# Kernel tuning notes

Hardware: AMD Instinct MI355X
Metric: run time of the kernel (lower is better)

Reference implementation:

```python
import jax, jax.numpy as jnp
import numpy as np

ALPHA = 0.1


def setup_inputs() -> dict:
    key = jax.random.key(0)
    ks = jax.random.split(key, 12)
    B, C, Q, XD, YD, E, H = 4, 256, 256, 64, 32, 64, 128
    inp = {
        "x": jax.random.normal(ks[0], (B, C, XD), jnp.float32),
        "y": jax.random.normal(ks[1], (B, C, YD), jnp.float32),
        "r_c": jax.random.normal(ks[2], (B, C, C, E), jnp.float32),
        "r_q": jax.random.normal(ks[3], (B, C, Q, E), jnp.float32),
        "c_att_map": jax.random.uniform(ks[4], (B, C, C), jnp.float32),
        "q_att_map": jax.random.uniform(ks[5], (B, Q, C), jnp.float32),
        "W1": jax.random.normal(ks[6], (XD + YD + E, H), jnp.float32) * 0.05,
        "b1": jnp.zeros((H,), jnp.float32),
        "W2": jax.random.normal(ks[7], (H, H), jnp.float32) * 0.05,
        "b2": jnp.zeros((H,), jnp.float32),
        "W3": jax.random.normal(ks[8], (H, E), jnp.float32) * 0.05,
        "b3": jnp.zeros((E,), jnp.float32),
    }
    return inp


def reference(x, y, r_c, r_q, c_att_map, q_att_map, W1, b1, W2, b2, W3, b3):
    B, C = r_c.shape[0], r_c.shape[1]
    # tile x,y across an outer C axis and concat with pairwise embeddings
    xx = jnp.broadcast_to(x[:, None, :, :], (B, C, C, x.shape[-1]))
    yy = jnp.broadcast_to(y[:, None, :, :], (B, C, C, y.shape[-1]))
    h = jnp.concatenate([xx, yy, r_c], axis=-1)          # [B,C,C,XD+YD+E]
    h = jax.nn.relu(h @ W1 + b1)
    h = jax.nn.relu(h @ W2 + b2)
    U = h @ W3 + b3                                       # [B,C,C,E]
    # delta[b,k,i,e] = sum_j c_att_map[b,i,j] * U[b,k,j,e]
    delta_r_c = jnp.einsum("bij,bkje->bkie", c_att_map, U)
    delta_r_q = jnp.einsum("bqj,bkje->bkqe", q_att_map, U)
    next_r_c = r_c - ALPHA * delta_r_c
    next_r_q = r_q - ALPHA * delta_r_q
    return (next_r_c, next_r_q)
```

## Files before the change

### kernel.cpp

```cpp
#include <hip/hip_runtime.h>
#include <hip/hip_bf16.h>

typedef __attribute__((ext_vector_type(8))) short  short8;
typedef __attribute__((ext_vector_type(4))) short  short4v;
typedef __attribute__((ext_vector_type(4))) float  f32x4;

#define ALPHA 0.1f

__device__ __forceinline__ unsigned short f2bf(float f) {
    unsigned int u = __float_as_uint(f);
    u = (u + 0x7FFFu + ((u >> 16) & 1u)) >> 16;
    return (unsigned short)u;
}

__device__ __forceinline__ f32x4 mfma16(short8 a, short8 b, f32x4 c) {
    return __builtin_amdgcn_mfma_f32_16x16x32_bf16(a, b, c, 0, 0, 0);
}

#define WS_P     0u
#define WS_W1RT  524288u
#define WS_W2T   540672u
#define WS_W3T   573440u
#define WS_ATTC  589824u
#define WS_ATTQ  1114112u

__global__ __launch_bounds__(256) void prep_kernel(
    const float* __restrict__ x, const float* __restrict__ y,
    const float* __restrict__ cat, const float* __restrict__ qat,
    const float* __restrict__ W1, const float* __restrict__ b1,
    const float* __restrict__ W2, const float* __restrict__ W3,
    unsigned char* __restrict__ ws)
{
    const unsigned int blk = blockIdx.x, tid = threadIdx.x;
    float* P = (float*)(ws + WS_P);
    unsigned short* W1rT = (unsigned short*)(ws + WS_W1RT);
    unsigned short* W2T  = (unsigned short*)(ws + WS_W2T);
    unsigned short* W3T  = (unsigned short*)(ws + WS_W3T);
    unsigned short* AC   = (unsigned short*)(ws + WS_ATTC);
    unsigned short* AQ   = (unsigned short*)(ws + WS_ATTQ);

    if (blk < 512u) {
        unsigned int t = blk * 256u + tid;
        unsigned int h = t & 127u, bj = t >> 7;
        float acc = b1[h];
        const float* xp = x + bj * 64u;
        const float* yp = y + bj * 32u;
        #pragma unroll 8
        for (int d = 0; d < 64; ++d) acc += xp[d] * W1[d * 128 + h];
        #pragma unroll 8
        for (int d = 0; d < 32; ++d) acc += yp[d] * W1[(64 + d) * 128 + h];
        P[t] = acc;
    } else if (blk < 544u) {
        unsigned int w = (blk - 512u) * 256u + tid;
        unsigned int h = w >> 6, e = w & 63u;
        W1rT[w] = f2bf(W1[(96u + e) * 128u + h]);
    } else if (blk < 608u) {
        unsigned int w = (blk - 544u) * 256u + tid;
        unsigned int n = w >> 7, k2 = w & 127u;
        W2T[w] = f2bf(W2[k2 * 128u + n]);
    } else if (blk < 640u) {
        unsigned int w = (blk - 608u) * 256u + tid;
        unsigned int e = w >> 7, h = w & 127u;
        W3T[w] = f2bf(W3[h * 64u + e]);
    } else if (blk < 896u) {
        unsigned int w = (blk - 640u) * 256u + tid;
        f32x4 v = *(const f32x4*)(cat + 4u * w);
        short4v o;
        #pragma unroll
        for (int i = 0; i < 4; ++i) o[i] = (short)f2bf(v[i]);
        *(short4v*)(AC + 4u * w) = o;
    } else {
        unsigned int w = (blk - 896u) * 256u + tid;
        f32x4 v = *(const f32x4*)(qat + 4u * w);
        short4v o;
        #pragma unroll
        for (int i = 0; i < 4; ++i) o[i] = (short)f2bf(v[i]);
        *(short4v*)(AQ + 4u * w) = o;
    }
}

__global__ __launch_bounds__(256) void fused_kernel(
    const float* __restrict__ rc, const float* __restrict__ rq,
    const float* __restrict__ b2, const float* __restrict__ b3,
    const unsigned char* __restrict__ ws,
    float* __restrict__ out_rc, float* __restrict__ out_rq)
{
    const float* P = (const float*)(ws + WS_P);
    const unsigned short* W1rT = (const unsigned short*)(ws + WS_W1RT);
    const unsigned short* W2T  = (const unsigned short*)(ws + WS_W2T);
    const unsigned short* W3T  = (const unsigned short*)(ws + WS_W3T);
    const unsigned short* AC   = (const unsigned short*)(ws + WS_ATTC);
    const unsigned short* AQ   = (const unsigned short*)(ws + WS_ATTQ);

    __shared__ unsigned short sH[64][136];
    __shared__ unsigned short sUT[64][264];

    const int tid  = threadIdx.x;
    const int lane = tid & 63;
    const int wid  = tid >> 6;
    const int l15  = lane & 15;
    const int lg   = lane >> 4;
    const int b    = blockIdx.y;
    const int k    = blockIdx.x;

    const size_t bk = (size_t)(b * 256 + k);
    const float* rcb = rc + bk * (256 * 64);
    const float* rqb = rq + bk * (256 * 64);
    const float* Pb  = P + b * (256 * 128);

    float b3v[4];
    #pragma unroll
    for (int ct = 0; ct < 4; ++ct) b3v[ct] = b3[16 * ct + l15];

    for (int jc = 0; jc < 4; ++jc) {
        const int jrow = jc * 64 + 16 * wid + l15;

        f32x4 accA[8];
        #pragma unroll
        for (int mt = 0; mt < 8; ++mt) accA[mt] = (f32x4)0.f;
        #pragma unroll
        for (int ks = 0; ks < 2; ++ks) {
            const float* ap = rcb + jrow * 64 + 32 * ks + 8 * lg;
            f32x4 a0 = *(const f32x4*)ap;
            f32x4 a1 = *(const f32x4*)(ap + 4);
            short8 bfrag;
            #pragma unroll
            for (int i = 0; i < 4; ++i) {
                bfrag[i]     = (short)f2bf(a0[i]);
                bfrag[4 + i] = (short)f2bf(a1[i]);
            }
            #pragma unroll
            for (int mt = 0; mt < 8; ++mt) {
                short8 afrag = *(const short8*)(W1rT + (16 * mt + l15) * 64 + 32 * ks + 8 * lg);
                accA[mt] = mfma16(afrag, bfrag, accA[mt]);
            }
        }
        #pragma unroll
        for (int mt = 0; mt < 8; ++mt) {
            f32x4 p4 = *(const f32x4*)(Pb + jrow * 128 + 16 * mt + 4 * lg);
            short4v o;
            #pragma unroll
            for (int r = 0; r < 4; ++r)
                o[r] = (short)f2bf(fmaxf(accA[mt][r] + p4[r], 0.f));
            *(short4v*)&sH[16 * wid + l15][16 * mt + 4 * lg] = o;
        }

        f32x4 accB[8];
        #pragma unroll
        for (int mt = 0; mt < 8; ++mt) accB[mt] = (f32x4)0.f;
        #pragma unroll
        for (int ks = 0; ks < 4; ++ks) {
            short8 bfrag = *(const short8*)(&sH[16 * wid + l15][32 * ks + 8 * lg]);
            #pragma unroll
            for (int mt = 0; mt < 8; ++mt) {
                short8 afrag = *(const short8*)(W2T + (16 * mt + l15) * 128 + 32 * ks + 8 * lg);
                accB[mt] = mfma16(afrag, bfrag, accB[mt]);
            }
        }
        #pragma unroll
        for (int mt = 0; mt < 8; ++mt) {
            f32x4 b2q = *(const f32x4*)(b2 + 16 * mt + 4 * lg);
            short4v o;
            #pragma unroll
            for (int r = 0; r < 4; ++r)
                o[r] = (short)f2bf(fmaxf(accB[mt][r] + b2q[r], 0.f));
            *(short4v*)&sH[16 * wid + l15][16 * mt + 4 * lg] = o;
        }

        f32x4 accC[4];
        #pragma unroll
        for (int ct = 0; ct < 4; ++ct) accC[ct] = (f32x4)0.f;
        #pragma unroll
        for (int ks = 0; ks < 4; ++ks) {
            short8 afrag = *(const short8*)(&sH[16 * wid + l15][32 * ks + 8 * lg]);
            #pragma unroll
            for (int ct = 0; ct < 4; ++ct) {
                short8 bfrag = *(const short8*)(W3T + (16 * ct + l15) * 128 + 32 * ks + 8 * lg);
                accC[ct] = mfma16(afrag, bfrag, accC[ct]);
            }
        }
        #pragma unroll
        for (int ct = 0; ct < 4; ++ct) {
            short4v o;
            #pragma unroll
            for (int r = 0; r < 4; ++r)
                o[r] = (short)f2bf(accC[ct][r] + b3v[ct]);
            *(short4v*)&sUT[16 * ct + l15][jc * 64 + 16 * wid + 4 * lg] = o;
        }
    }

    __syncthreads();

    const unsigned short* amap[2] = { AC + b * 65536, AQ + b * 65536 };
    const float* src[2]           = { rcb, rqb };
    float* dst[2] = { out_rc + bk * 16384, out_rq + bk * 16384 };
    const int i0 = 64 * wid;

    #pragma unroll
    for (int p = 0; p < 2; ++p) {
        f32x4 acc[4][4];
        #pragma unroll
        for (int et = 0; et < 4; ++et)
            #pragma unroll
            for (int it = 0; it < 4; ++it) acc[et][it] = (f32x4)0.f;
        for (int ks = 0; ks < 8; ++ks) {
            short8 uf[4];
            #pragma unroll
            for (int et = 0; et < 4; ++et)
                uf[et] = *(const short8*)(&sUT[16 * et + l15][32 * ks + 8 * lg]);
            #pragma unroll
            for (int it = 0; it < 4; ++it) {
                short8 af = *(const short8*)(amap[p] + (i0 + 16 * it + l15) * 256 + 32 * ks + 8 * lg);
                #pragma unroll
                for (int et = 0; et < 4; ++et)
                    acc[et][it] = mfma16(uf[et], af, acc[et][it]);
            }
        }
        #pragma unroll
        for (int it = 0; it < 4; ++it) {
            #pragma unroll
            for (int et = 0; et < 4; ++et) {
                const int i = i0 + 16 * it + l15;
                const int e0 = 16 * et + 4 * lg;
                f32x4 rv = *(const f32x4*)(src[p] + i * 64 + e0);
                f32x4 o;
                #pragma unroll
                for (int r = 0; r < 4; ++r)
                    o[r] = rv[r] - ALPHA * acc[et][it][r];
                *(f32x4*)(dst[p] + i * 64 + e0) = o;
            }
        }
    }
}

extern "C" void kernel_launch(void* const* d_in, const int* in_sizes, int n_in,
                              void* d_out, int out_size, void* d_ws, size_t ws_size,
                              hipStream_t stream)
{
    const float* x   = (const float*)d_in[0];
    const float* y   = (const float*)d_in[1];
    const float* rc  = (const float*)d_in[2];
    const float* rq  = (const float*)d_in[3];
    const float* cat = (const float*)d_in[4];
    const float* qat = (const float*)d_in[5];
    const float* W1  = (const float*)d_in[6];
    const float* b1  = (const float*)d_in[7];
    const float* W2  = (const float*)d_in[8];
    const float* b2  = (const float*)d_in[9];
    const float* W3  = (const float*)d_in[10];
    const float* b3  = (const float*)d_in[11];

    float* out_rc = (float*)d_out;
    float* out_rq = out_rc + (size_t)4 * 256 * 256 * 64;
    unsigned char* ws = (unsigned char*)d_ws;

    prep_kernel<<<1152, 256, 0, stream>>>(x, y, cat, qat, W1, b1, W2, W3, ws);
    fused_kernel<<<dim3(256, 4), 256, 0, stream>>>(rc, rq, b2, b3, ws, out_rc, out_rq);
}
```

Measured before the change: 373.4 us.

## Split fused MLP+attention kernel into separate MLP and attention kernels

Splits the fused per-(b,k) kernel into an MLP kernel, one block per 64-row j-chunk, that writes U transposed in bf16 to workspace, and an attention kernel with one block per (map, b, k). This exposes more independent blocks, removes the serial jc loop and the large shared U buffer, and should raise occupancy. The cost is an extra global round-trip for U, read twice, and one additional kernel launch.

```diff
diff --git a/kernel.cpp b/kernel.cpp
--- a/kernel.cpp
+++ b/kernel.cpp
@@ -23,6 +23,7 @@
 #define WS_W3T   573440u
 #define WS_ATTC  589824u
 #define WS_ATTQ  1114112u
+#define WS_UT    1638400u
 
 __global__ __launch_bounds__(256) void prep_kernel(
     const float* __restrict__ x, const float* __restrict__ y,
@@ -79,156 +80,166 @@
     }
 }
 
-__global__ __launch_bounds__(256) void fused_kernel(
-    const float* __restrict__ rc, const float* __restrict__ rq,
-    const float* __restrict__ b2, const float* __restrict__ b3,
-    const unsigned char* __restrict__ ws,
-    float* __restrict__ out_rc, float* __restrict__ out_rq)
+__global__ __launch_bounds__(256) void mlp_kernel(
+    const float* __restrict__ rc, const float* __restrict__ b2,
+    const float* __restrict__ b3, unsigned char* __restrict__ ws)
 {
     const float* P = (const float*)(ws + WS_P);
     const unsigned short* W1rT = (const unsigned short*)(ws + WS_W1RT);
     const unsigned short* W2T  = (const unsigned short*)(ws + WS_W2T);
     const unsigned short* W3T  = (const unsigned short*)(ws + WS_W3T);
-    const unsigned short* AC   = (const unsigned short*)(ws + WS_ATTC);
-    const unsigned short* AQ   = (const unsigned short*)(ws + WS_ATTQ);
+    unsigned short* UT = (unsigned short*)(ws + WS_UT);
 
     __shared__ unsigned short sH[64][136];
-    __shared__ unsigned short sUT[64][264];
 
     const int tid  = threadIdx.x;
     const int lane = tid & 63;
     const int wid  = tid >> 6;
     const int l15  = lane & 15;
     const int lg   = lane >> 4;
-    const int b    = blockIdx.y;
-    const int k    = blockIdx.x;
-
-    const size_t bk = (size_t)(b * 256 + k);
-    const float* rcb = rc + bk * (256 * 64);
-    const float* rqb = rq + bk * (256 * 64);
+    const int jc   = blockIdx.x;
+    const int bk   = blockIdx.y;
+    const int b    = bk >> 8;
+
+    const float* rcb = rc + (size_t)bk * (256 * 64);
     const float* Pb  = P + b * (256 * 128);
+    unsigned short* UTb = UT + (size_t)bk * 16384;
+
+    const int jrow = jc * 64 + 16 * wid + l15;
+
+    f32x4 accA[8];
+    #pragma unroll
+    for (int mt = 0; mt < 8; ++mt) accA[mt] = (f32x4)0.f;
+    #pragma unroll
+    for (int ks = 0; ks < 2; ++ks) {
+        const float* ap = rcb + jrow * 64 + 32 * ks + 8 * lg;
+        f32x4 a0 = *(const f32x4*)ap;
+        f32x4 a1 = *(const f32x4*)(ap + 4);
+        short8 bfrag;
+        #pragma unroll
+        for (int i = 0; i < 4; ++i) {
+            bfrag[i]     = (short)f2bf(a0[i]);
+            bfrag[4 + i] = (short)f2bf(a1[i]);
+        }
+        #pragma unroll
+        for (int mt = 0; mt < 8; ++mt) {
+            short8 afrag = *(const short8*)(W1rT + (16 * mt + l15) * 64 + 32 * ks + 8 * lg);
+            accA[mt] = mfma16(afrag, bfrag, accA[mt]);
+        }
+    }
+    #pragma unroll
+    for (int mt = 0; mt < 8; ++mt) {
+        f32x4 p4 = *(const f32x4*)(Pb + jrow * 128 + 16 * mt + 4 * lg);
+        short4v o;
+        #pragma unroll
+        for (int r = 0; r < 4; ++r)
+            o[r] = (short)f2bf(fmaxf(accA[mt][r] + p4[r], 0.f));
+        *(short4v*)&sH[16 * wid + l15][16 * mt + 4 * lg] = o;
+    }
+
+    f32x4 accB[8];
+    #pragma unroll
+    for (int mt = 0; mt < 8; ++mt) accB[mt] = (f32x4)0.f;
+    #pragma unroll
+    for (int ks = 0; ks < 4; ++ks) {
+        short8 bfrag = *(const short8*)(&sH[16 * wid + l15][32 * ks + 8 * lg]);
+        #pragma unroll
+        for (int mt = 0; mt < 8; ++mt) {
+            short8 afrag = *(const short8*)(W2T + (16 * mt + l15) * 128 + 32 * ks + 8 * lg);
+            accB[mt] = mfma16(afrag, bfrag, accB[mt]);
+        }
+    }
+    #pragma unroll
+    for (int mt = 0; mt < 8; ++mt) {
+        f32x4 b2q = *(const f32x4*)(b2 + 16 * mt + 4 * lg);
+        short4v o;
+        #pragma unroll
+        for (int r = 0; r < 4; ++r)
+            o[r] = (short)f2bf(fmaxf(accB[mt][r] + b2q[r], 0.f));
+        *(short4v*)&sH[16 * wid + l15][16 * mt + 4 * lg] = o;
+    }
 
     float b3v[4];
     #pragma unroll
     for (int ct = 0; ct < 4; ++ct) b3v[ct] = b3[16 * ct + l15];
-
-    for (int jc = 0; jc < 4; ++jc) {
-        const int jrow = jc * 64 + 16 * wid + l15;
-
-        f32x4 accA[8];
-        #pragma unroll
-        for (int mt = 0; mt < 8; ++mt) accA[mt] = (f32x4)0.f;
-        #pragma unroll
-        for (int ks = 0; ks < 2; ++ks) {
-            const float* ap = rcb + jrow * 64 + 32 * ks + 8 * lg;
-            f32x4 a0 = *(const f32x4*)ap;
-            f32x4 a1 = *(const f32x4*)(ap + 4);
-            short8 bfrag;
+    f32x4 accC[4];
+    #pragma unroll
+    for (int ct = 0; ct < 4; ++ct) accC[ct] = (f32x4)0.f;
+    #pragma unroll
+    for (int ks = 0; ks < 4; ++ks) {
+        short8 afrag = *(const short8*)(&sH[16 * wid + l15][32 * ks + 8 * lg]);
+        #pragma unroll
+        for (int ct = 0; ct < 4; ++ct) {
+            short8 bfrag = *(const short8*)(W3T + (16 * ct + l15) * 128 + 32 * ks + 8 * lg);
+            accC[ct] = mfma16(afrag, bfrag, accC[ct]);
+        }
+    }
+    #pragma unroll
+    for (int ct = 0; ct < 4; ++ct) {
+        short4v o;
+        #pragma unroll
+        for (int r = 0; r < 4; ++r)
+            o[r] = (short)f2bf(accC[ct][r] + b3v[ct]);
+        *(short4v*)(UTb + (16 * ct + l15) * 256 + jc * 64 + 16 * wid + 4 * lg) = o;
+    }
+}
+
+__global__ __launch_bounds__(256) void att_kernel(
+    const float* __restrict__ rc, const float* __restrict__ rq,
+    const unsigned char* __restrict__ ws,
+    float* __restrict__ out_rc, float* __restrict__ out_rq)
+{
+    const unsigned short* AC = (const unsigned short*)(ws + WS_ATTC);
+    const unsigned short* AQ = (const unsigned short*)(ws + WS_ATTQ);
+    const unsigned short* UT = (const unsigned short*)(ws + WS_UT);
+
+    const int tid  = threadIdx.x;
+    const int lane = tid & 63;
+    const int wid  = tid >> 6;
+    const int l15  = lane & 15;
+    const int lg   = lane >> 4;
+    const int p    = blockIdx.x;
+    const int bk   = blockIdx.y;
+    const int b    = bk >> 8;
+
+    const unsigned short* UTb = UT + (size_t)bk * 16384;
+    const unsigned short* amap = (p == 0 ? AC : AQ) + b * 65536;
+    const float* src = (p == 0 ? rc : rq) + (size_t)bk * 16384;
+    float* dst = (p == 0 ? out_rc : out_rq) + (size_t)bk * 16384;
+
+    const int i0 = 64 * wid;
+
+    f32x4 acc[4][4];
+    #pragma unroll
+    for (int et = 0; et < 4; ++et)
+        #pragma unroll
+        for (int it = 0; it < 4; ++it) acc[et][it] = (f32x4)0.f;
+
+    for (int ks = 0; ks < 8; ++ks) {
+        short8 uf[4];
+        #pragma unroll
+        for (int et = 0; et < 4; ++et)
+            uf[et] = *(const short8*)(UTb + (16 * et + l15) * 256 + 32 * ks + 8 * lg);
+        #pragma unroll
+        for (int it = 0; it < 4; ++it) {
+            short8 af = *(const short8*)(amap + (i0 + 16 * it + l15) * 256 + 32 * ks + 8 * lg);
             #pragma unroll
-            for (int i = 0; i < 4; ++i) {
-                bfrag[i]     = (short)f2bf(a0[i]);
-                bfrag[4 + i] = (short)f2bf(a1[i]);
-            }
-            #pragma unroll
-            for (int mt = 0; mt < 8; ++mt) {
-                short8 afrag = *(const short8*)(W1rT + (16 * mt + l15) * 64 + 32 * ks + 8 * lg);
-                accA[mt] = mfma16(afrag, bfrag, accA[mt]);
-            }
-        }
-        #pragma unroll
-        for (int mt = 0; mt < 8; ++mt) {
-            f32x4 p4 = *(const f32x4*)(Pb + jrow * 128 + 16 * mt + 4 * lg);
-            short4v o;
+            for (int et = 0; et < 4; ++et)
+                acc[et][it] = mfma16(uf[et], af, acc[et][it]);
+        }
+    }
+    #pragma unroll
+    for (int it = 0; it < 4; ++it) {
+        #pragma unroll
+        for (int et = 0; et < 4; ++et) {
+            const int i = i0 + 16 * it + l15;
+            const int e0 = 16 * et + 4 * lg;
+            f32x4 rv = *(const f32x4*)(src + i * 64 + e0);
+            f32x4 o;
             #pragma unroll
             for (int r = 0; r < 4; ++r)
-                o[r] = (short)f2bf(fmaxf(accA[mt][r] + p4[r], 0.f));
-            *(short4v*)&sH[16 * wid + l15][16 * mt + 4 * lg] = o;
-        }
-
-        f32x4 accB[8];
-        #pragma unroll
-        for (int mt = 0; mt < 8; ++mt) accB[mt] = (f32x4)0.f;
-        #pragma unroll
-        for (int ks = 0; ks < 4; ++ks) {
-            short8 bfrag = *(const short8*)(&sH[16 * wid + l15][32 * ks + 8 * lg]);
-            #pragma unroll
-            for (int mt = 0; mt < 8; ++mt) {
-                short8 afrag = *(const short8*)(W2T + (16 * mt + l15) * 128 + 32 * ks + 8 * lg);
-                accB[mt] = mfma16(afrag, bfrag, accB[mt]);
-            }
-        }
-        #pragma unroll
-        for (int mt = 0; mt < 8; ++mt) {
-            f32x4 b2q = *(const f32x4*)(b2 + 16 * mt + 4 * lg);
-            short4v o;
-            #pragma unroll
-            for (int r = 0; r < 4; ++r)
-                o[r] = (short)f2bf(fmaxf(accB[mt][r] + b2q[r], 0.f));
-            *(short4v*)&sH[16 * wid + l15][16 * mt + 4 * lg] = o;
-        }
-
-        f32x4 accC[4];
-        #pragma unroll
-        for (int ct = 0; ct < 4; ++ct) accC[ct] = (f32x4)0.f;
-        #pragma unroll
-        for (int ks = 0; ks < 4; ++ks) {
-            short8 afrag = *(const short8*)(&sH[16 * wid + l15][32 * ks + 8 * lg]);
-            #pragma unroll
-            for (int ct = 0; ct < 4; ++ct) {
-                short8 bfrag = *(const short8*)(W3T + (16 * ct + l15) * 128 + 32 * ks + 8 * lg);
-                accC[ct] = mfma16(afrag, bfrag, accC[ct]);
-            }
-        }
-        #pragma unroll
-        for (int ct = 0; ct < 4; ++ct) {
-            short4v o;
-            #pragma unroll
-            for (int r = 0; r < 4; ++r)
-                o[r] = (short)f2bf(accC[ct][r] + b3v[ct]);
-            *(short4v*)&sUT[16 * ct + l15][jc * 64 + 16 * wid + 4 * lg] = o;
-        }
-    }
-
-    __syncthreads();
-
-    const unsigned short* amap[2] = { AC + b * 65536, AQ + b * 65536 };
-    const float* src[2]           = { rcb, rqb };
-    float* dst[2] = { out_rc + bk * 16384, out_rq + bk * 16384 };
-    const int i0 = 64 * wid;
-
-    #pragma unroll
-    for (int p = 0; p < 2; ++p) {
-        f32x4 acc[4][4];
-        #pragma unroll
-        for (int et = 0; et < 4; ++et)
-            #pragma unroll
-            for (int it = 0; it < 4; ++it) acc[et][it] = (f32x4)0.f;
-        for (int ks = 0; ks < 8; ++ks) {
-            short8 uf[4];
-            #pragma unroll
-            for (int et = 0; et < 4; ++et)
-                uf[et] = *(const short8*)(&sUT[16 * et + l15][32 * ks + 8 * lg]);
-            #pragma unroll
-            for (int it = 0; it < 4; ++it) {
-                short8 af = *(const short8*)(amap[p] + (i0 + 16 * it + l15) * 256 + 32 * ks + 8 * lg);
-                #pragma unroll
-                for (int et = 0; et < 4; ++et)
-                    acc[et][it] = mfma16(uf[et], af, acc[et][it]);
-            }
-        }
-        #pragma unroll
-        for (int it = 0; it < 4; ++it) {
-            #pragma unroll
-            for (int et = 0; et < 4; ++et) {
-                const int i = i0 + 16 * it + l15;
-                const int e0 = 16 * et + 4 * lg;
-                f32x4 rv = *(const f32x4*)(src[p] + i * 64 + e0);
-                f32x4 o;
-                #pragma unroll
-                for (int r = 0; r < 4; ++r)
-                    o[r] = rv[r] - ALPHA * acc[et][it][r];
-                *(f32x4*)(dst[p] + i * 64 + e0) = o;
-            }
+                o[r] = rv[r] - ALPHA * acc[et][it][r];
+            *(f32x4*)(dst + i * 64 + e0) = o;
         }
     }
 }
@@ -255,5 +266,6 @@
     unsigned char* ws = (unsigned char*)d_ws;
 
     prep_kernel<<<1152, 256, 0, stream>>>(x, y, cat, qat, W1, b1, W2, W3, ws);
-    fused_kernel<<<dim3(256, 4), 256, 0, stream>>>(rc, rq, b2, b3, ws, out_rc, out_rq);
-}
+    mlp_kernel<<<dim3(4, 1024), 256, 0, stream>>>(rc, b2, b3, ws);
+    att_kernel<<<dim3(2, 1024), 256, 0, stream>>>(rc, rq, ws, out_rc, out_rq);
+}
```

Measured after the change: 474.4 us. 1.27x slower.
